# Optimization experiments

Measured on AMD Instinct MI355X. Metric: run time of the kernel, lower is better.

Reference implementation:

```python
import jax, jax.numpy as jnp
import numpy as np

EPS = 1e-5


def _ligru_layer(x, W, U, gamma, beta):
    """One bidirectional LiGRU layer. x: (B,T,F) -> (B,T,2H)."""
    B = x.shape[0]
    H = U.shape[1]
    # bidirectional: stack forward copy and time-flipped copy along batch
    x2 = jnp.concatenate([x, x[:, ::-1]], axis=0)  # (2B, T, F)
    w = jnp.einsum('btf,gf->btg', x2, W)           # (2B, T, 2H)
    # training-mode BatchNorm1d over flattened (2B*T, 2H), biased variance
    flat = w.reshape(-1, w.shape[-1])
    mean = flat.mean(axis=0)
    var = flat.var(axis=0)
    w = (w - mean) * jax.lax.rsqrt(var + EPS) * gamma + beta

    def step(h, wt):
        gates = wt + h @ U.T            # (2B, 2H)
        at, zt = gates[:, :H], gates[:, H:]
        z = jax.nn.sigmoid(zt)
        h = z * h + (1.0 - z) * jax.nn.relu(at)
        return h, h

    h0 = jnp.zeros((w.shape[0], H), dtype=w.dtype)
    _, hs = jax.lax.scan(step, h0, jnp.swapaxes(w, 0, 1))  # (T, 2B, H)
    hs = jnp.swapaxes(hs, 0, 1)                            # (2B, T, H)
    h_f, h_b = hs[:B], hs[B:, ::-1]                        # un-flip backward dir
    return jnp.concatenate([h_f, h_b], axis=2)             # (B, T, 2H)


def setup_inputs() -> dict:
    key = jax.random.key(0)
    ks = jax.random.split(key, 9)
    B, T, F, H = 16, 500, 512, 1024
    return {
        'x': jax.random.normal(ks[0], (B, T, F), jnp.float32),
        'w0': jax.random.normal(ks[1], (2 * H, F), jnp.float32) * (1.0 / np.sqrt(F)),
        'u0': jax.random.normal(ks[2], (2 * H, H), jnp.float32) * (1.0 / np.sqrt(H)),
        'g0': jax.random.uniform(ks[3], (2 * H,), jnp.float32, 0.5, 1.5),
        'b0': jax.random.normal(ks[4], (2 * H,), jnp.float32) * 0.1,
        'w1': jax.random.normal(ks[5], (2 * H, 2 * H), jnp.float32) * (1.0 / np.sqrt(2 * H)),
        'u1': jax.random.normal(ks[6], (2 * H, H), jnp.float32) * (1.0 / np.sqrt(H)),
        'g1': jax.random.uniform(ks[7], (2 * H,), jnp.float32, 0.5, 1.5),
        'b1': jax.random.normal(ks[8], (2 * H,), jnp.float32) * 0.1,
    }


def reference(x, w0, u0, g0, b0, w1, u1, g1, b1):
    h = _ligru_layer(x, w0, u0, g0, b0)   # (B, T, 2H)
    h = _ligru_layer(h, w1, u1, g1, b1)   # (B, T, 2H)
    return h
```

## Files before the change

### kernel.cpp

```cpp
#include <hip/hip_runtime.h>
#include <stdint.h>

#define KT 500
#define KH 1024
#define KG 2048

typedef short bf16x8 __attribute__((ext_vector_type(8)));
typedef float f32x4 __attribute__((ext_vector_type(4)));

__device__ __forceinline__ unsigned short f2bf(float f){
  union { float f; unsigned int i; } u; u.f = f;
  unsigned int x = u.i;
  return (unsigned short)((x + 0x7fffu + ((x >> 16) & 1u)) >> 16);
}
__device__ __forceinline__ float bf2f(unsigned short h){
  union { unsigned int i; float f; } u; u.i = ((unsigned int)h) << 16;
  return u.f;
}

template<int OFF>
__device__ __forceinline__ void load_b128_dev_off(uint4& dst, const void* p){
  asm volatile("global_load_dwordx4 %0, %1, off offset:%c2 sc1"
               : "=v"(dst) : "v"(p), "i"(OFF) : "memory");
}
__device__ __forceinline__ void store_b32_dev(void* p, unsigned int v){
  asm volatile("global_store_dword %0, %1, off sc1"
               :: "v"(p), "v"(v) : "memory");
}
__device__ __forceinline__ void wait_vm0(){
  asm volatile("s_waitcnt vmcnt(0)" ::: "memory");
}

__global__ __launch_bounds__(256) void castk(const float* __restrict__ s,
                                             unsigned short* __restrict__ d, int n4){
  int i = blockIdx.x*256 + threadIdx.x;
  if (i >= n4) return;
  float4 v = ((const float4*)s)[i];
  unsigned int lo = (unsigned int)f2bf(v.x) | ((unsigned int)f2bf(v.y) << 16);
  unsigned int hi = (unsigned int)f2bf(v.z) | ((unsigned int)f2bf(v.w) << 16);
  ((uint2*)d)[i] = make_uint2(lo, hi);
}

template<int MODE, int KDIM>
__global__ __launch_bounds__(256) void gemm_bn(
    const unsigned short* __restrict__ A,
    const unsigned short* __restrict__ Bw,
    unsigned short* __restrict__ Wout)
{
  __shared__ __attribute__((aligned(16))) unsigned short As[128*72];
  __shared__ __attribute__((aligned(16))) unsigned short Bs[128*72];
  const int tid = threadIdx.x;
  const int lane = tid & 63, wid = tid >> 6;
  const int ntile = blockIdx.x, mtile = blockIdx.y;
  const int arow_loc = tid >> 3;
  const int k8 = tid & 7;

  long abaseLo[4], abaseHi[4], bbase[4];
  #pragma unroll
  for (int i = 0; i < 4; i++){
    int r = mtile*128 + i*32 + arow_loc;
    int s = r / KT;
    int t = r - s*KT;
    if (MODE == 0){
      abaseLo[i] = (s < 16) ? (long)((s*KT + t)*512)
                            : (long)(((s-16)*KT + (KT-1-t))*512);
      abaseHi[i] = 0;
    } else {
      int sp = s & 15;
      int rev = (s >= 16);
      abaseLo[i] = (long)((sp*KT + (rev ? KT-1-t : t)) * KH);
      abaseHi[i] = (long)(((16+sp)*KT + (rev ? t : KT-1-t)) * KH);
    }
    bbase[i] = (long)(ntile*128 + i*32 + arow_loc) * KDIM;
  }

  f32x4 acc[4][4];
  #pragma unroll
  for (int a=0;a<4;a++)
    #pragma unroll
    for (int b=0;b<4;b++)
      acc[a][b] = (f32x4){0.f,0.f,0.f,0.f};

  const int mhalf = wid & 1, nhalf = wid >> 1;
  const int lrow = lane & 15, quad = lane >> 4;

  for (int k0 = 0; k0 < KDIM; k0 += 64){
    const int kel = k0 + k8*8;
    #pragma unroll
    for (int i = 0; i < 4; i++){
      long aoff;
      if (MODE == 0) aoff = abaseLo[i] + kel;
      else           aoff = (kel < KH) ? (abaseLo[i] + kel) : (abaseHi[i] + (kel - KH));
      uint4 va = *(const uint4*)(A + aoff);
      uint4 vb = *(const uint4*)(Bw + bbase[i] + kel);
      *(uint4*)&As[(i*32 + arow_loc)*72 + k8*8] = va;
      *(uint4*)&Bs[(i*32 + arow_loc)*72 + k8*8] = vb;
    }
    __syncthreads();
    #pragma unroll
    for (int kk = 0; kk < 64; kk += 32){
      bf16x8 af[4], bfr[4];
      #pragma unroll
      for (int mt=0; mt<4; mt++)
        af[mt] = *(const bf16x8*)&As[(mhalf*64 + mt*16 + lrow)*72 + kk + quad*8];
      #pragma unroll
      for (int nt=0; nt<4; nt++)
        bfr[nt] = *(const bf16x8*)&Bs[(nhalf*64 + nt*16 + lrow)*72 + kk + quad*8];
      #pragma unroll
      for (int mt=0; mt<4; mt++)
        #pragma unroll
        for (int nt=0; nt<4; nt++)
          acc[mt][nt] = __builtin_amdgcn_mfma_f32_16x16x32_bf16(af[mt], bfr[nt], acc[mt][nt], 0, 0, 0);
    }
    __syncthreads();
  }

  #pragma unroll
  for (int mt=0; mt<4; mt++)
    #pragma unroll
    for (int nt=0; nt<4; nt++)
      #pragma unroll
      for (int r=0; r<4; r++){
        int grow = mtile*128 + mhalf*64 + mt*16 + quad*4 + r;
        int gcol = ntile*128 + nhalf*64 + nt*16 + lrow;
        Wout[(long)grow*KG + gcol] = f2bf(acc[mt][nt][r]);
      }
}

__global__ __launch_bounds__(256) void bn_partial(const unsigned short* __restrict__ W,
                                                  float* __restrict__ part){
  const int blk = blockIdx.x, tid = threadIdx.x;
  const int c0 = tid*8;
  float s[8], qq[8];
  #pragma unroll
  for (int j=0;j<8;j++){ s[j]=0.f; qq[j]=0.f; }
  const unsigned short* base = W + (long)blk*128*KG + c0;
  for (int r=0;r<128;r++){
    uint4 v = *(const uint4*)(base + (long)r*KG);
    unsigned int w[4] = {v.x, v.y, v.z, v.w};
    #pragma unroll
    for (int p=0;p<4;p++){
      union { unsigned int i; float f; } lo, hi;
      lo.i = w[p] << 16;
      hi.i = w[p] & 0xffff0000u;
      s[2*p]   += lo.f; qq[2*p]   += lo.f*lo.f;
      s[2*p+1] += hi.f; qq[2*p+1] += hi.f*hi.f;
    }
  }
  float* pd = part + (long)blk*4096;
  #pragma unroll
  for (int j=0;j<8;j++){ pd[c0+j] = s[j]; pd[KG + c0 + j] = qq[j]; }
}

__global__ __launch_bounds__(256) void bn_final(const float* __restrict__ part,
                                                const float* __restrict__ gamma,
                                                const float* __restrict__ beta,
                                                float* __restrict__ scsh){
  int g = blockIdx.x*256 + threadIdx.x;
  float s=0.f, qq=0.f;
  for (int b=0;b<125;b++){ s += part[(long)b*4096 + g]; qq += part[(long)b*4096 + KG + g]; }
  float mean = s * (1.f/16000.f);
  float var  = qq * (1.f/16000.f) - mean*mean;
  float sc = gamma[g] * rsqrtf(var + 1e-5f);
  scsh[g]      = sc;
  scsh[KG + g] = beta[g] - mean*sc;
}

template<int LAYER>
__global__ __launch_bounds__(256, 1) void recur(
    const unsigned short* __restrict__ Ub,
    const unsigned short* __restrict__ Wn,
    const float* __restrict__ scsh,
    unsigned short* __restrict__ hbuf,
    int* __restrict__ flags,
    unsigned short* __restrict__ hsOut,
    float* __restrict__ out)
{
  __shared__ float gA[32*20];
  __shared__ float gZ[32*20];

  const int tid = threadIdx.x;
  const int q = blockIdx.x;
  const int ga = q*16;
  const int lane = tid & 63, wid = tid >> 6;
  const int lrow = lane & 15, quad = lane >> 4;
  const int m = wid & 1, kh = wid >> 1;
  const int es = tid >> 3, ep = tid & 7;

  bf16x8 ufA[16], ufZ[16];
  {
    const unsigned short* ua = Ub + (long)(ga + lrow)*KH + kh*512 + quad*8;
    const unsigned short* uz = ua + (long)KH*KH;
    #pragma unroll
    for (int c=0;c<16;c++){
      ufA[c] = *(const bf16x8*)(ua + c*32);
      ufZ[c] = *(const bf16x8*)(uz + c*32);
    }
  }

  float2 scav = *(const float2*)&scsh[ga + 2*ep];
  float2 shav = *(const float2*)&scsh[KG + ga + 2*ep];
  float2 sczv = *(const float2*)&scsh[KH + ga + 2*ep];
  float2 shzv = *(const float2*)&scsh[KG + KH + ga + 2*ep];
  float2 hprev = make_float2(0.f, 0.f);

  const long aoff = (long)(m*16 + lrow)*KH + kh*512 + quad*8;
  const unsigned short* hb0 = hbuf + aoff;
  const unsigned short* hb1 = hbuf + 32768 + aoff;

  for (int t = 0; t < KT; t++){
    const unsigned short* wr = Wn + (long)(es*KT + t)*KG + ga + 2*ep;
    unsigned int wa01 = *(const unsigned int*)(wr);
    unsigned int wz01 = *(const unsigned int*)(wr + KH);
    asm volatile("" ::: "memory");

    if (t > 0){
      const int fl = (t-1)*64 + kh*32 + (lane & 31);
      while (__hip_atomic_load(&flags[fl], __ATOMIC_RELAXED,
                               __HIP_MEMORY_SCOPE_AGENT) == 0){}
    }

    const unsigned short* hb = (t & 1) ? hb1 : hb0;
    uint4 af[16];
    #define LDAF(i) load_b128_dev_off<(i)*64>(af[i], hb)
    LDAF(0);  LDAF(1);  LDAF(2);  LDAF(3);
    LDAF(4);  LDAF(5);  LDAF(6);  LDAF(7);
    LDAF(8);  LDAF(9);  LDAF(10); LDAF(11);
    LDAF(12); LDAF(13); LDAF(14); LDAF(15);
    #undef LDAF
    wait_vm0();
    __builtin_amdgcn_sched_barrier(0);

    f32x4 aA0 = (f32x4){0,0,0,0}, aA1 = aA0, aZ0 = aA0, aZ1 = aA0;
    #pragma unroll
    for (int c=0;c<16;c+=2){
      bf16x8 x0 = *(bf16x8*)&af[c];
      bf16x8 x1 = *(bf16x8*)&af[c+1];
      aA0 = __builtin_amdgcn_mfma_f32_16x16x32_bf16(x0, ufA[c],   aA0, 0,0,0);
      aZ0 = __builtin_amdgcn_mfma_f32_16x16x32_bf16(x0, ufZ[c],   aZ0, 0,0,0);
      aA1 = __builtin_amdgcn_mfma_f32_16x16x32_bf16(x1, ufA[c+1], aA1, 0,0,0);
      aZ1 = __builtin_amdgcn_mfma_f32_16x16x32_bf16(x1, ufZ[c+1], aZ1, 0,0,0);
    }
    f32x4 accA = aA0 + aA1;
    f32x4 accZ = aZ0 + aZ1;

    if (kh){
      #pragma unroll
      for (int r=0;r<4;r++){
        gA[(m*16 + quad*4 + r)*20 + lrow] = accA[r];
        gZ[(m*16 + quad*4 + r)*20 + lrow] = accZ[r];
      }
    }
    __syncthreads();
    if (!kh){
      #pragma unroll
      for (int r=0;r<4;r++){
        int ix = (m*16 + quad*4 + r)*20 + lrow;
        gA[ix] += accA[r];
        gZ[ix] += accZ[r];
      }
    }
    __syncthreads();

    float2 gav = *(const float2*)&gA[es*20 + 2*ep];
    float2 gzv = *(const float2*)&gZ[es*20 + 2*ep];
    float aa0 = gav.x + bf2f((unsigned short)(wa01 & 0xffff)) * scav.x + shav.x;
    float aa1 = gav.y + bf2f((unsigned short)(wa01 >> 16))    * scav.y + shav.y;
    float zz0 = gzv.x + bf2f((unsigned short)(wz01 & 0xffff)) * sczv.x + shzv.x;
    float zz1 = gzv.y + bf2f((unsigned short)(wz01 >> 16))    * sczv.y + shzv.y;
    float z0 = 1.f/(1.f + __expf(-zz0));
    float z1 = 1.f/(1.f + __expf(-zz1));
    float hn0 = z0*hprev.x + (1.f - z0)*fmaxf(aa0, 0.f);
    float hn1 = z1*hprev.y + (1.f - z1)*fmaxf(aa1, 0.f);
    hprev = make_float2(hn0, hn1);

    unsigned int hpack = (unsigned int)f2bf(hn0) | ((unsigned int)f2bf(hn1) << 16);
    store_b32_dev(hbuf + ((t+1)&1)*32768 + es*KH + ga + 2*ep, hpack);
    wait_vm0();
    __syncthreads();
    if (tid == 0)
      __hip_atomic_store(&flags[t*64 + q], 1, __ATOMIC_RELAXED, __HIP_MEMORY_SCOPE_AGENT);

    if (LAYER == 0){
      *(unsigned int*)&hsOut[(long)(es*KT + t)*KH + ga + 2*ep] = hpack;
    } else {
      if (es < 16)
        *(float2*)&out[(long)(es*KT + t)*KG + ga + 2*ep] = make_float2(hn0, hn1);
      else
        *(float2*)&out[(long)((es-16)*KT + (KT-1-t))*KG + KH + ga + 2*ep] = make_float2(hn0, hn1);
    }
  }
}

extern "C" void kernel_launch(void* const* d_in, const int* in_sizes, int n_in,
                              void* d_out, int out_size, void* d_ws, size_t ws_size,
                              hipStream_t stream)
{
  const float* x  = (const float*)d_in[0];
  const float* w0 = (const float*)d_in[1];
  const float* u0 = (const float*)d_in[2];
  const float* g0 = (const float*)d_in[3];
  const float* b0 = (const float*)d_in[4];
  const float* w1 = (const float*)d_in[5];
  const float* u1 = (const float*)d_in[6];
  const float* g1 = (const float*)d_in[7];
  const float* b1 = (const float*)d_in[8];
  float* out = (float*)d_out;

  char* p = (char*)d_ws;
  auto alloc = [&](size_t n){ char* r = p; p += (n + 255) & ~(size_t)255; return r; };
  unsigned short* xb   = (unsigned short*)alloc((size_t)16*KT*512*2);
  unsigned short* w0b  = (unsigned short*)alloc((size_t)KG*512*2);
  unsigned short* u0b  = (unsigned short*)alloc((size_t)KG*KH*2);
  unsigned short* w1b  = (unsigned short*)alloc((size_t)KG*KG*2);
  unsigned short* u1b  = (unsigned short*)alloc((size_t)KG*KH*2);
  unsigned short* wbuf = (unsigned short*)alloc((size_t)32*KT*KG*2);
  unsigned short* hs0  = (unsigned short*)alloc((size_t)32*KT*KH*2);
  float* part          = (float*)alloc((size_t)125*4096*4);
  float* scsh          = (float*)alloc((size_t)2*KG*4);
  unsigned short* hbuf = (unsigned short*)alloc((size_t)2*2*32*KH*2);
  int* flags           = (int*)alloc((size_t)2*KT*64*4);

  auto cast = [&](const float* s, unsigned short* d, int n){
    int n4 = n >> 2;
    castk<<<(n4+255)/256, 256, 0, stream>>>(s, d, n4);
  };
  cast(x,  xb,  16*KT*512);
  cast(w0, w0b, KG*512);
  cast(u0, u0b, KG*KH);
  cast(w1, w1b, KG*KG);
  cast(u1, u1b, KG*KH);
  hipMemsetAsync(hbuf,  0, (size_t)2*2*32*KH*2, stream);
  hipMemsetAsync(flags, 0, (size_t)2*KT*64*4,  stream);

  gemm_bn<0,512><<<dim3(16,125), 256, 0, stream>>>(xb, w0b, wbuf);
  bn_partial<<<125,256,0,stream>>>(wbuf, part);
  bn_final<<<8,256,0,stream>>>(part, g0, b0, scsh);
  recur<0><<<64,256,0,stream>>>(u0b, wbuf, scsh, hbuf, flags, hs0, (float*)nullptr);

  gemm_bn<1,2048><<<dim3(16,125), 256, 0, stream>>>(hs0, w1b, wbuf);
  bn_partial<<<125,256,0,stream>>>(wbuf, part);
  bn_final<<<8,256,0,stream>>>(part, g1, b1, scsh);
  recur<1><<<64,256,0,stream>>>(u1b, wbuf, scsh, hbuf + 2*32*KH, flags + KT*64,
                                (unsigned short*)nullptr, out);
}
```

Baseline: 5.225 ms.

## Streamline recurrent-step grid sync with monotonic padded flags and split load waits

Each block now has one padded monotonic counter flag, set to t+1, instead of a fresh flag per timestep. Only 32 lanes poll these flags. The h loads are consumed in two halves, so the first half of the MFMAs starts after vmcnt(8). The second __syncthreads in the gate reduction is removed by writing both K-halves to separate shared buffers and summing on read. The output store now comes before the h broadcast store, the U fragments are pinned to AGPRs, and the aim is to shorten the per-step critical path of this latency-bound cross-block recurrence.

Measured after the change: 4.263 ms. -18.4%, faster.

```diff
diff --git a/kernel.cpp b/kernel.cpp
--- a/kernel.cpp
+++ b/kernel.cpp
@@ -4,6 +4,7 @@
 #define KT 500
 #define KH 1024
 #define KG 2048
+#define FPAD 16
 
 typedef short bf16x8 __attribute__((ext_vector_type(8)));
 typedef float f32x4 __attribute__((ext_vector_type(4)));
@@ -29,6 +30,9 @@
 }
 __device__ __forceinline__ void wait_vm0(){
   asm volatile("s_waitcnt vmcnt(0)" ::: "memory");
+}
+__device__ __forceinline__ void wait_vm8(){
+  asm volatile("s_waitcnt vmcnt(8)" ::: "memory");
 }
 
 __global__ __launch_bounds__(256) void castk(const float* __restrict__ s,
@@ -176,8 +180,10 @@
     unsigned short* __restrict__ hsOut,
     float* __restrict__ out)
 {
-  __shared__ float gA[32*20];
-  __shared__ float gZ[32*20];
+  __shared__ float gA0[32*20];
+  __shared__ float gZ0[32*20];
+  __shared__ float gA1[32*20];
+  __shared__ float gZ1[32*20];
 
   const int tid = threadIdx.x;
   const int q = blockIdx.x;
@@ -194,7 +200,9 @@
     #pragma unroll
     for (int c=0;c<16;c++){
       ufA[c] = *(const bf16x8*)(ua + c*32);
+      asm volatile("" : "+a"(ufA[c]));
       ufZ[c] = *(const bf16x8*)(uz + c*32);
+      asm volatile("" : "+a"(ufZ[c]));
     }
   }
 
@@ -215,9 +223,13 @@
     asm volatile("" ::: "memory");
 
     if (t > 0){
-      const int fl = (t-1)*64 + kh*32 + (lane & 31);
-      while (__hip_atomic_load(&flags[fl], __ATOMIC_RELAXED,
-                               __HIP_MEMORY_SCOPE_AGENT) == 0){}
+      if (lane < 32){
+        const int* fp = &flags[(kh*32 + lane) << 4];
+        while (__hip_atomic_load(fp, __ATOMIC_RELAXED,
+                                 __HIP_MEMORY_SCOPE_AGENT) < t){}
+      }
+    } else {
+      wait_vm0();
     }
 
     const unsigned short* hb = (t & 1) ? hb1 : hb0;
@@ -228,12 +240,13 @@
     LDAF(8);  LDAF(9);  LDAF(10); LDAF(11);
     LDAF(12); LDAF(13); LDAF(14); LDAF(15);
     #undef LDAF
-    wait_vm0();
+
+    f32x4 aA0 = (f32x4){0,0,0,0}, aA1 = aA0, aZ0 = aA0, aZ1 = aA0;
+
+    wait_vm8();
     __builtin_amdgcn_sched_barrier(0);
-
-    f32x4 aA0 = (f32x4){0,0,0,0}, aA1 = aA0, aZ0 = aA0, aZ1 = aA0;
-    #pragma unroll
-    for (int c=0;c<16;c+=2){
+    #pragma unroll
+    for (int c=0;c<8;c+=2){
       bf16x8 x0 = *(bf16x8*)&af[c];
       bf16x8 x1 = *(bf16x8*)&af[c+1];
       aA0 = __builtin_amdgcn_mfma_f32_16x16x32_bf16(x0, ufA[c],   aA0, 0,0,0);
@@ -241,33 +254,39 @@
       aA1 = __builtin_amdgcn_mfma_f32_16x16x32_bf16(x1, ufA[c+1], aA1, 0,0,0);
       aZ1 = __builtin_amdgcn_mfma_f32_16x16x32_bf16(x1, ufZ[c+1], aZ1, 0,0,0);
     }
+    wait_vm0();
+    __builtin_amdgcn_sched_barrier(0);
+    #pragma unroll
+    for (int c=8;c<16;c+=2){
+      bf16x8 x0 = *(bf16x8*)&af[c];
+      bf16x8 x1 = *(bf16x8*)&af[c+1];
+      aA0 = __builtin_amdgcn_mfma_f32_16x16x32_bf16(x0, ufA[c],   aA0, 0,0,0);
+      aZ0 = __builtin_amdgcn_mfma_f32_16x16x32_bf16(x0, ufZ[c],   aZ0, 0,0,0);
+      aA1 = __builtin_amdgcn_mfma_f32_16x16x32_bf16(x1, ufA[c+1], aA1, 0,0,0);
+      aZ1 = __builtin_amdgcn_mfma_f32_16x16x32_bf16(x1, ufZ[c+1], aZ1, 0,0,0);
+    }
     f32x4 accA = aA0 + aA1;
     f32x4 accZ = aZ0 + aZ1;
 
-    if (kh){
+    {
+      float* gAd = kh ? gA1 : gA0;
+      float* gZd = kh ? gZ1 : gZ0;
       #pragma unroll
       for (int r=0;r<4;r++){
-        gA[(m*16 + quad*4 + r)*20 + lrow] = accA[r];
-        gZ[(m*16 + quad*4 + r)*20 + lrow] = accZ[r];
+        gAd[(m*16 + quad*4 + r)*20 + lrow] = accA[r];
+        gZd[(m*16 + quad*4 + r)*20 + lrow] = accZ[r];
       }
     }
     __syncthreads();
-    if (!kh){
-      #pragma unroll
-      for (int r=0;r<4;r++){
-        int ix = (m*16 + quad*4 + r)*20 + lrow;
-        gA[ix] += accA[r];
-        gZ[ix] += accZ[r];
-      }
-    }
-    __syncthreads();
-
-    float2 gav = *(const float2*)&gA[es*20 + 2*ep];
-    float2 gzv = *(const float2*)&gZ[es*20 + 2*ep];
-    float aa0 = gav.x + bf2f((unsigned short)(wa01 & 0xffff)) * scav.x + shav.x;
-    float aa1 = gav.y + bf2f((unsigned short)(wa01 >> 16))    * scav.y + shav.y;
-    float zz0 = gzv.x + bf2f((unsigned short)(wz01 & 0xffff)) * sczv.x + shzv.x;
-    float zz1 = gzv.y + bf2f((unsigned short)(wz01 >> 16))    * sczv.y + shzv.y;
+
+    float2 ga0 = *(const float2*)&gA0[es*20 + 2*ep];
+    float2 ga1 = *(const float2*)&gA1[es*20 + 2*ep];
+    float2 gz0 = *(const float2*)&gZ0[es*20 + 2*ep];
+    float2 gz1 = *(const float2*)&gZ1[es*20 + 2*ep];
+    float aa0 = ga0.x + ga1.x + bf2f((unsigned short)(wa01 & 0xffff)) * scav.x + shav.x;
+    float aa1 = ga0.y + ga1.y + bf2f((unsigned short)(wa01 >> 16))    * scav.y + shav.y;
+    float zz0 = gz0.x + gz1.x + bf2f((unsigned short)(wz01 & 0xffff)) * sczv.x + shzv.x;
+    float zz1 = gz0.y + gz1.y + bf2f((unsigned short)(wz01 >> 16))    * sczv.y + shzv.y;
     float z0 = 1.f/(1.f + __expf(-zz0));
     float z1 = 1.f/(1.f + __expf(-zz1));
     float hn0 = z0*hprev.x + (1.f - z0)*fmaxf(aa0, 0.f);
@@ -275,11 +294,6 @@
     hprev = make_float2(hn0, hn1);
 
     unsigned int hpack = (unsigned int)f2bf(hn0) | ((unsigned int)f2bf(hn1) << 16);
-    store_b32_dev(hbuf + ((t+1)&1)*32768 + es*KH + ga + 2*ep, hpack);
-    wait_vm0();
-    __syncthreads();
-    if (tid == 0)
-      __hip_atomic_store(&flags[t*64 + q], 1, __ATOMIC_RELAXED, __HIP_MEMORY_SCOPE_AGENT);
 
     if (LAYER == 0){
       *(unsigned int*)&hsOut[(long)(es*KT + t)*KH + ga + 2*ep] = hpack;
@@ -289,6 +303,13 @@
       else
         *(float2*)&out[(long)((es-16)*KT + (KT-1-t))*KG + KH + ga + 2*ep] = make_float2(hn0, hn1);
     }
+
+    store_b32_dev(hbuf + ((t+1)&1)*32768 + es*KH + ga + 2*ep, hpack);
+    wait_vm0();
+    __syncthreads();
+    if (tid == 0)
+      __hip_atomic_store(&flags[q << 4], t + 1, __ATOMIC_RELAXED,
+                         __HIP_MEMORY_SCOPE_AGENT);
   }
 }
 
@@ -319,7 +340,7 @@
   float* part          = (float*)alloc((size_t)125*4096*4);
   float* scsh          = (float*)alloc((size_t)2*KG*4);
   unsigned short* hbuf = (unsigned short*)alloc((size_t)2*2*32*KH*2);
-  int* flags           = (int*)alloc((size_t)2*KT*64*4);
+  int* flags           = (int*)alloc((size_t)2*64*FPAD*4);
 
   auto cast = [&](const float* s, unsigned short* d, int n){
     int n4 = n >> 2;
@@ -331,7 +352,7 @@
   cast(w1, w1b, KG*KG);
   cast(u1, u1b, KG*KH);
   hipMemsetAsync(hbuf,  0, (size_t)2*2*32*KH*2, stream);
-  hipMemsetAsync(flags, 0, (size_t)2*KT*64*4,  stream);
+  hipMemsetAsync(flags, 0, (size_t)2*64*FPAD*4, stream);
 
   gemm_bn<0,512><<<dim3(16,125), 256, 0, stream>>>(xb, w0b, wbuf);
   bn_partial<<<125,256,0,stream>>>(wbuf, part);
@@ -341,6 +362,6 @@
   gemm_bn<1,2048><<<dim3(16,125), 256, 0, stream>>>(hs0, w1b, wbuf);
   bn_partial<<<125,256,0,stream>>>(wbuf, part);
   bn_final<<<8,256,0,stream>>>(part, g1, b1, scsh);
-  recur<1><<<64,256,0,stream>>>(u1b, wbuf, scsh, hbuf + 2*32*KH, flags + KT*64,
+  recur<1><<<64,256,0,stream>>>(u1b, wbuf, scsh, hbuf + 2*32*KH, flags + 64*FPAD,
                                 (unsigned short*)nullptr, out);
 }
```
